# Performance work log

Hardware: AMD Instinct MI355X
Metric: run time of the kernel (lower is better)

Reference implementation:

```python
import jax, jax.numpy as jnp
import numpy as np

B, N, C, R = 4, 4096, 64, 16
EPS = 1e-12


def setup_inputs() -> dict:
    key = jax.random.key(0)
    k_x, k_w, k_u = jax.random.split(key, 3)
    x = jax.random.normal(k_x, (B, N, C), dtype=jnp.float32)
    W = jax.random.uniform(k_w, (B, N, N), dtype=jnp.float32)
    # lazily-initialized learnable low-rank factor U ~ 0.01 * randn(N, r)
    U = 0.01 * jax.random.normal(k_u, (N, R), dtype=jnp.float32)
    w_scale = jnp.asarray(1.0, dtype=jnp.float32)
    return {"x": x, "W": W, "U": U, "w_scale": w_scale}


def reference(x, W, U, w_scale):
    # symmetrize adjacency: W <- (W + W^T)/2
    Ws = 0.5 * (W + jnp.swapaxes(W, -1, -2))            # [B,N,N]
    # low-rank symmetric gate A = sigmoid(U U^T), shared over batch
    A = jax.nn.sigmoid(U @ U.T)                          # [N,N]
    K = Ws * A[None, :, :]                               # [B,N,N]
    # degree normalization K <- D^{-1/2} K D^{-1/2}
    # (diag_embed + two bmms in the original == row/col broadcast scaling)
    deg = jnp.maximum(K.sum(axis=-1), EPS)               # [B,N]
    d = jax.lax.rsqrt(deg)                               # [B,N]
    K = K * d[:, :, None] * d[:, None, :]                # [B,N,N]
    # coupling: w_scale * K @ x
    return w_scale * jnp.einsum('bnm,bmc->bnc', K, x)    # [B,N,C]
```

## Files before the change

### kernel.cpp

```cpp
#include <hip/hip_runtime.h>
#include <hip/hip_bf16.h>

#define B_ 4
#define N_ 4096
#define C_ 64
#define R_ 16
#define EPS_ 1e-12f

typedef __attribute__((ext_vector_type(8))) short bf16x8;
typedef __attribute__((ext_vector_type(4))) float f32x4;

static __device__ __forceinline__ unsigned short f2bf(float f) {
    unsigned int u = __float_as_uint(f);
    unsigned int r = (u + 0x7fffu + ((u >> 16) & 1u)) >> 16;
    return (unsigned short)r;
}
static __device__ __forceinline__ float bf2f(unsigned short us) {
    return __uint_as_float(((unsigned int)us) << 16);
}

static __device__ __forceinline__ size_t k0f_off(int b, int rt, int k32, int fq, int fr) {
    return ((((size_t)(b * 256 + rt)) * 128 + k32) * 4 + fq) * 128 + fr * 8;
}

__global__ __launch_bounds__(256) void k_pass1(
    const float* __restrict__ W, const float* __restrict__ U,
    unsigned short* __restrict__ K0, float* __restrict__ deg)
{
    const int tj = blockIdx.x, ti = blockIdx.y;
    if (ti > tj) return;
    const int I = ti * 64, J = tj * 64;
    const bool diag = (ti == tj);
    const int t = threadIdx.x;
    const int ii = t >> 2, g = t & 3, jjg = g * 16;

    __shared__ float UJ[64][17];
    __shared__ float Wc[64][65];
    __shared__ __align__(16) unsigned short K0s[64][72];

    {
        const float4 v = *(const float4*)(U + (size_t)(J + (t >> 2)) * R_ + (t & 3) * 4);
        UJ[t >> 2][(t & 3) * 4 + 0] = v.x;
        UJ[t >> 2][(t & 3) * 4 + 1] = v.y;
        UJ[t >> 2][(t & 3) * 4 + 2] = v.z;
        UJ[t >> 2][(t & 3) * 4 + 3] = v.w;
    }

    float4 wcv[4], wrv[4], wcvN[4], wrvN[4];
    #pragma unroll
    for (int k = 0; k < 4; k++) {
        const int idx = t + 256 * k, row = idx >> 4, c4 = idx & 15;
        wcv[k] = *(const float4*)(W + ((size_t)(0 * N_ + J + row)) * N_ + I + c4 * 4);
    }
    #pragma unroll
    for (int h = 0; h < 4; h++)
        wrv[h] = *(const float4*)(W + ((size_t)(0 * N_ + I + ii)) * N_ + J + jjg + 4 * h);

    float ui[16];
    {
        const float* up = U + (size_t)(I + ii) * R_;
        #pragma unroll
        for (int h = 0; h < 4; h++) {
            float4 v = *(const float4*)(up + 4 * h);
            ui[4*h] = v.x; ui[4*h+1] = v.y; ui[4*h+2] = v.z; ui[4*h+3] = v.w;
        }
    }
    __syncthreads();

    float a[16];
    #pragma unroll
    for (int q = 0; q < 16; q++) {
        float s = 0.f;
        #pragma unroll
        for (int k = 0; k < 16; k++) s += ui[k] * UJ[jjg + q][k];
        a[q] = 1.0f / (1.0f + __expf(-s));
    }

    #pragma unroll
    for (int k = 0; k < 4; k++) {
        const int idx = t + 256 * k, row = idx >> 4, c4 = idx & 15;
        Wc[row][c4*4+0] = wcv[k].x; Wc[row][c4*4+1] = wcv[k].y;
        Wc[row][c4*4+2] = wcv[k].z; Wc[row][c4*4+3] = wcv[k].w;
    }
    __syncthreads();

    for (int b = 0; b < B_; b++) {
        if (b < B_ - 1) {
            #pragma unroll
            for (int k = 0; k < 4; k++) {
                const int idx = t + 256 * k, row = idx >> 4, c4 = idx & 15;
                wcvN[k] = *(const float4*)(W + ((size_t)((b+1) * N_ + J + row)) * N_ + I + c4 * 4);
            }
            #pragma unroll
            for (int h = 0; h < 4; h++)
                wrvN[h] = *(const float4*)(W + ((size_t)((b+1) * N_ + I + ii)) * N_ + J + jjg + 4 * h);
        }

        const float* wrf = (const float*)wrv;
        float sumI = 0.f;
        unsigned int pk[8];
        #pragma unroll
        for (int q = 0; q < 16; q++) {
            float k0 = 0.5f * (wrf[q] + Wc[jjg + q][ii]) * a[q];
            sumI += k0;
            unsigned short us = f2bf(k0);
            if (q & 1) pk[q >> 1] |= ((unsigned int)us) << 16;
            else       pk[q >> 1] = us;
        }
        *(int4*)(&K0s[ii][jjg])     = make_int4(pk[0], pk[1], pk[2], pk[3]);
        *(int4*)(&K0s[ii][jjg + 8]) = make_int4(pk[4], pk[5], pk[6], pk[7]);
        {
            const int rt  = (I + ii) >> 4, fr = ii & 15;
            const int k32 = (J >> 5) + (g >> 1), fqa = (g & 1) * 2;
            unsigned short* dst = K0 + k0f_off(b, rt, k32, fqa, fr);
            *(int4*)(dst)       = make_int4(pk[0], pk[1], pk[2], pk[3]);
            *(int4*)(dst + 128) = make_int4(pk[4], pk[5], pk[6], pk[7]);
        }
        {
            float s = sumI + __shfl_xor(sumI, 1, 64);
            s += __shfl_xor(s, 2, 64);
            if (g == 0) atomicAdd(deg + b * N_ + I + ii, s);
        }
        __syncthreads();

        if (!diag) {
            const int c2 = t & 31, r8 = t >> 5;
            unsigned int v[8];
            float cs0 = 0.f, cs1 = 0.f;
            #pragma unroll
            for (int k = 0; k < 8; k++) {
                v[k] = *(const unsigned int*)(&K0s[r8 * 8 + k][c2 * 2]);
                cs0 += bf2f((unsigned short)(v[k] & 0xffffu));
                cs1 += bf2f((unsigned short)(v[k] >> 16));
            }
            unsigned int plo[4], phi[4];
            #pragma unroll
            for (int m = 0; m < 4; m++) {
                plo[m] = (v[2*m] & 0xffffu) | (v[2*m+1] << 16);
                phi[m] = (v[2*m] >> 16) | (v[2*m+1] & 0xffff0000u);
            }
            const int rtp  = (J >> 4) + (c2 >> 3), fr0 = (2 * c2) & 15;
            const int k32p = (I >> 5) + (r8 >> 2), fqp = r8 & 3;
            unsigned short* dst0 = K0 + k0f_off(b, rtp, k32p, fqp, fr0);
            *(int4*)(dst0)     = make_int4(plo[0], plo[1], plo[2], plo[3]);
            *(int4*)(dst0 + 8) = make_int4(phi[0], phi[1], phi[2], phi[3]);
            cs0 += __shfl_xor(cs0, 32, 64);
            cs1 += __shfl_xor(cs1, 32, 64);
            if ((t & 32) == 0) {
                atomicAdd(deg + b * N_ + J + 2 * c2,     cs0);
                atomicAdd(deg + b * N_ + J + 2 * c2 + 1, cs1);
            }
        }
        if (b < B_ - 1) {
            #pragma unroll
            for (int k = 0; k < 4; k++) {
                const int idx = t + 256 * k, row = idx >> 4, c4 = idx & 15;
                Wc[row][c4*4+0] = wcvN[k].x; Wc[row][c4*4+1] = wcvN[k].y;
                Wc[row][c4*4+2] = wcvN[k].z; Wc[row][c4*4+3] = wcvN[k].w;
            }
            #pragma unroll
            for (int h = 0; h < 4; h++) wrv[h] = wrvN[h];
            __syncthreads();
        }
    }
}

__global__ __launch_bounds__(256) void k_xdT(
    const float* __restrict__ x, const float* __restrict__ deg,
    unsigned short* __restrict__ xdT)
{
    const int jt = blockIdx.x, b = blockIdx.y;
    const int J = jt * 64, t = threadIdx.x;
    __shared__ float xt[64][69];
    #pragma unroll
    for (int k = 0; k < 4; k++) {
        int idx = t + 256 * k;
        int row = idx >> 4, f4 = idx & 15;
        float d = rsqrtf(fmaxf(deg[b * N_ + J + row], EPS_));
        float4 v = *(const float4*)(x + ((size_t)(b * N_ + J + row)) * C_ + f4 * 4);
        xt[row][f4*4+0] = v.x * d; xt[row][f4*4+1] = v.y * d;
        xt[row][f4*4+2] = v.z * d; xt[row][f4*4+3] = v.w * d;
    }
    __syncthreads();
    #pragma unroll
    for (int p = 0; p < 2; p++) {
        const int linear = p * 256 + t;
        const int k32h = linear >> 8, rem = linear & 255;
        const int cg = rem >> 6, l = rem & 63, fq = l >> 4, fr = l & 15;
        const int c = cg * 16 + fr;
        const int jb = k32h * 32 + fq * 8;
        unsigned int pk[4];
        #pragma unroll
        for (int m = 0; m < 4; m++) {
            pk[m] = (unsigned int)f2bf(xt[jb + 2*m][c]) |
                    ((unsigned int)f2bf(xt[jb + 2*m + 1][c]) << 16);
        }
        unsigned short* dst = xdT +
            (((size_t)(b * 128 + (J >> 5) + k32h)) * 4 + cg) * 512 + l * 8;
        *(int4*)dst = make_int4(pk[0], pk[1], pk[2], pk[3]);
    }
}

static __device__ __forceinline__ void gll16(const unsigned short* g, const unsigned short* l) {
    __builtin_amdgcn_global_load_lds(
        (const __attribute__((address_space(1))) unsigned int*)g,
        (__attribute__((address_space(3))) unsigned int*)l,
        16, 0, 0);
}

__global__ __launch_bounds__(256, 2) void k_gemm(
    const unsigned short* __restrict__ K0, const unsigned short* __restrict__ xdT,
    const float* __restrict__ deg, const float* __restrict__ wsc_p,
    float* __restrict__ out)
{
    const int mg = blockIdx.x, b = blockIdx.y;
    const int t = threadIdx.x, w = t >> 6, lane = t & 63;
    const int rt0 = mg * 2;
    const int rtl = w & 1, cgp = (w >> 1) * 2;
    const int fq = lane >> 4, fr = lane & 15;
    const int rt = rt0 + rtl;

    __shared__ __align__(16) unsigned short As[2 * 8 * 512];
    __shared__ __align__(16) unsigned short Bs[2 * 16 * 512];

    const float wsc = wsc_p[0];
    float dsc[4];
    #pragma unroll
    for (int r = 0; r < 4; r++)
        dsc[r] = wsc * rsqrtf(fmaxf(deg[b * N_ + rt * 16 + fq * 4 + r], EPS_));

    const unsigned short* gp[6];
    const unsigned short* lp[6];
    int ginc[6], linc[6];
    #pragma unroll
    for (int j = 0; j < 6; j++) {
        const int id = w * 6 + j;
        if (id < 8) {
            const int art = id >> 2, c = id & 3;
            gp[j] = K0 + (((size_t)(b * 256 + rt0 + art)) * 128 + c) * 512 + lane * 8;
            lp[j] = As + id * 512;
            ginc[j] = 4 * 512;
            linc[j] = 8 * 512;
        } else {
            const int bi = id - 8, kc = bi >> 2, cg = bi & 3;
            gp[j] = xdT + (((size_t)(b * 128 + kc)) * 4 + cg) * 512 + lane * 8;
            lp[j] = Bs + bi * 512;
            ginc[j] = 4 * 2048;
            linc[j] = 16 * 512;
        }
    }

    asm volatile("s_waitcnt vmcnt(0)" ::: "memory");
    __builtin_amdgcn_sched_barrier(0);

    #pragma unroll
    for (int j = 0; j < 6; j++) {
        gll16(gp[j], lp[j]);
        gp[j] += ginc[j];
    }

    f32x4 acc0 = {0.f,0.f,0.f,0.f}, acc1 = {0.f,0.f,0.f,0.f};
    const int lo = lane * 8;
    int cur = 0;

    for (int t4 = 0; t4 < 32; t4++) {
        if (t4 < 31) {
            #pragma unroll
            for (int j = 0; j < 6; j++) {
                gll16(gp[j], lp[j] + (cur ? 0 : linc[j]));
                gp[j] += ginc[j];
            }
        }
        __builtin_amdgcn_sched_barrier(0);
        if (t4 < 31) asm volatile("s_waitcnt vmcnt(6)" ::: "memory");
        else         asm volatile("s_waitcnt vmcnt(0)" ::: "memory");
        __builtin_amdgcn_s_barrier();
        __builtin_amdgcn_sched_barrier(0);

        const unsigned short* Ab = As + (cur ? 8 * 512 : 0) + rtl * 4 * 512 + lo;
        const unsigned short* Bb = Bs + (cur ? 16 * 512 : 0) + cgp * 512 + lo;
        #pragma unroll
        for (int c = 0; c < 4; c++) {
            bf16x8 av = *(const bf16x8*)(Ab + c * 512);
            bf16x8 b0 = *(const bf16x8*)(Bb + c * 2048);
            bf16x8 b1 = *(const bf16x8*)(Bb + c * 2048 + 512);
            acc0 = __builtin_amdgcn_mfma_f32_16x16x32_bf16(av, b0, acc0, 0, 0, 0);
            acc1 = __builtin_amdgcn_mfma_f32_16x16x32_bf16(av, b1, acc1, 0, 0, 0);
        }
        __builtin_amdgcn_sched_barrier(0);
        __builtin_amdgcn_s_barrier();
        cur ^= 1;
    }

    #pragma unroll
    for (int r = 0; r < 4; r++) {
        const int row = rt * 16 + fq * 4 + r;
        float* op = out + ((size_t)(b * N_ + row)) * C_;
        op[cgp * 16 + fr]      = dsc[r] * acc0[r];
        op[cgp * 16 + 16 + fr] = dsc[r] * acc1[r];
    }
}

extern "C" void kernel_launch(void* const* d_in, const int* in_sizes, int n_in,
                              void* d_out, int out_size, void* d_ws, size_t ws_size,
                              hipStream_t stream)
{
    const float* x   = (const float*)d_in[0];
    const float* W   = (const float*)d_in[1];
    const float* U   = (const float*)d_in[2];
    const float* wsc = (const float*)d_in[3];
    float* out = (float*)d_out;

    unsigned short* K0  = (unsigned short*)d_ws;
    float*          deg = (float*)((char*)d_ws + (size_t)B_ * N_ * N_ * 2);
    unsigned short* xdT = (unsigned short*)((char*)deg + (size_t)B_ * N_ * 4);

    hipMemsetAsync(deg, 0, (size_t)B_ * N_ * sizeof(float), stream);
    hipLaunchKernelGGL(k_pass1, dim3(64, 64), dim3(256), 0, stream, W, U, K0, deg);
    hipLaunchKernelGGL(k_xdT,  dim3(64, 4),   dim3(256), 0, stream, x, deg, xdT);
    hipLaunchKernelGGL(k_gemm, dim3(128, 4),  dim3(256), 0, stream, K0, xdT, deg, wsc, out);
}
```

Before: 444.8 us.

## Launch only upper-triangle tiles and double-buffer shared tiles to drop a barrier

Replaces the 64x64 grid with early-exiting lower-triangle blocks by a linear grid of 2080 blocks, mapped to (ti,tj) via a triangular index inversion. The transposed W tile in shared memory becomes bf16 and is double-buffered along with the K0 staging tile, so the next batch's tile is written before the single barrier and the second per-iteration __syncthreads is removed. The aims are less wasted block scheduling, fewer barriers per batch and a smaller shared footprint that allows higher occupancy. The trade-off is that the transposed W values are rounded to bf16 before symmetrization, adding some precision loss.

```diff
diff --git a/kernel.cpp b/kernel.cpp
--- a/kernel.cpp
+++ b/kernel.cpp
@@ -27,16 +27,20 @@
     const float* __restrict__ W, const float* __restrict__ U,
     unsigned short* __restrict__ K0, float* __restrict__ deg)
 {
-    const int tj = blockIdx.x, ti = blockIdx.y;
-    if (ti > tj) return;
+    const int lin = blockIdx.x;
+    float ff = 64.5f - sqrtf(64.5f * 64.5f - 2.0f * (float)lin);
+    int ti = (int)ff;
+    while ((ti + 1) * (129 - (ti + 1)) / 2 <= lin) ti++;
+    while (ti * (129 - ti) / 2 > lin) ti--;
+    const int tj = ti + (lin - ti * (129 - ti) / 2);
     const int I = ti * 64, J = tj * 64;
     const bool diag = (ti == tj);
     const int t = threadIdx.x;
     const int ii = t >> 2, g = t & 3, jjg = g * 16;
 
     __shared__ float UJ[64][17];
-    __shared__ float Wc[64][65];
-    __shared__ __align__(16) unsigned short K0s[64][72];
+    __shared__ unsigned short Wc[2][64][66];
+    __shared__ __align__(16) unsigned short K0s[2][64][72];
 
     {
         const float4 v = *(const float4*)(U + (size_t)(J + (t >> 2)) * R_ + (t & 3) * 4);
@@ -79,12 +83,15 @@
     #pragma unroll
     for (int k = 0; k < 4; k++) {
         const int idx = t + 256 * k, row = idx >> 4, c4 = idx & 15;
-        Wc[row][c4*4+0] = wcv[k].x; Wc[row][c4*4+1] = wcv[k].y;
-        Wc[row][c4*4+2] = wcv[k].z; Wc[row][c4*4+3] = wcv[k].w;
+        unsigned int d0 = (unsigned int)f2bf(wcv[k].x) | ((unsigned int)f2bf(wcv[k].y) << 16);
+        unsigned int d1 = (unsigned int)f2bf(wcv[k].z) | ((unsigned int)f2bf(wcv[k].w) << 16);
+        *(unsigned int*)&Wc[0][row][c4 * 4]     = d0;
+        *(unsigned int*)&Wc[0][row][c4 * 4 + 2] = d1;
     }
     __syncthreads();
 
     for (int b = 0; b < B_; b++) {
+        const int cur = b & 1;
         if (b < B_ - 1) {
             #pragma unroll
             for (int k = 0; k < 4; k++) {
@@ -101,14 +108,14 @@
         unsigned int pk[8];
         #pragma unroll
         for (int q = 0; q < 16; q++) {
-            float k0 = 0.5f * (wrf[q] + Wc[jjg + q][ii]) * a[q];
+            float k0 = 0.5f * (wrf[q] + bf2f(Wc[cur][jjg + q][ii])) * a[q];
             sumI += k0;
             unsigned short us = f2bf(k0);
             if (q & 1) pk[q >> 1] |= ((unsigned int)us) << 16;
             else       pk[q >> 1] = us;
         }
-        *(int4*)(&K0s[ii][jjg])     = make_int4(pk[0], pk[1], pk[2], pk[3]);
-        *(int4*)(&K0s[ii][jjg + 8]) = make_int4(pk[4], pk[5], pk[6], pk[7]);
+        *(int4*)(&K0s[cur][ii][jjg])     = make_int4(pk[0], pk[1], pk[2], pk[3]);
+        *(int4*)(&K0s[cur][ii][jjg + 8]) = make_int4(pk[4], pk[5], pk[6], pk[7]);
         {
             const int rt  = (I + ii) >> 4, fr = ii & 15;
             const int k32 = (J >> 5) + (g >> 1), fqa = (g & 1) * 2;
@@ -121,6 +128,18 @@
             s += __shfl_xor(s, 2, 64);
             if (g == 0) atomicAdd(deg + b * N_ + I + ii, s);
         }
+        if (b < B_ - 1) {
+            #pragma unroll
+            for (int k = 0; k < 4; k++) {
+                const int idx = t + 256 * k, row = idx >> 4, c4 = idx & 15;
+                unsigned int d0 = (unsigned int)f2bf(wcvN[k].x) | ((unsigned int)f2bf(wcvN[k].y) << 16);
+                unsigned int d1 = (unsigned int)f2bf(wcvN[k].z) | ((unsigned int)f2bf(wcvN[k].w) << 16);
+                *(unsigned int*)&Wc[cur ^ 1][row][c4 * 4]     = d0;
+                *(unsigned int*)&Wc[cur ^ 1][row][c4 * 4 + 2] = d1;
+            }
+            #pragma unroll
+            for (int h = 0; h < 4; h++) wrv[h] = wrvN[h];
+        }
         __syncthreads();
 
         if (!diag) {
@@ -129,7 +148,7 @@
             float cs0 = 0.f, cs1 = 0.f;
             #pragma unroll
             for (int k = 0; k < 8; k++) {
-                v[k] = *(const unsigned int*)(&K0s[r8 * 8 + k][c2 * 2]);
+                v[k] = *(const unsigned int*)(&K0s[cur][r8 * 8 + k][c2 * 2]);
                 cs0 += bf2f((unsigned short)(v[k] & 0xffffu));
                 cs1 += bf2f((unsigned short)(v[k] >> 16));
             }
@@ -150,17 +169,6 @@
                 atomicAdd(deg + b * N_ + J + 2 * c2,     cs0);
                 atomicAdd(deg + b * N_ + J + 2 * c2 + 1, cs1);
             }
-        }
-        if (b < B_ - 1) {
-            #pragma unroll
-            for (int k = 0; k < 4; k++) {
-                const int idx = t + 256 * k, row = idx >> 4, c4 = idx & 15;
-                Wc[row][c4*4+0] = wcvN[k].x; Wc[row][c4*4+1] = wcvN[k].y;
-                Wc[row][c4*4+2] = wcvN[k].z; Wc[row][c4*4+3] = wcvN[k].w;
-            }
-            #pragma unroll
-            for (int h = 0; h < 4; h++) wrv[h] = wrvN[h];
-            __syncthreads();
         }
     }
 }
@@ -316,7 +324,7 @@
     unsigned short* xdT = (unsigned short*)((char*)deg + (size_t)B_ * N_ * 4);
 
     hipMemsetAsync(deg, 0, (size_t)B_ * N_ * sizeof(float), stream);
-    hipLaunchKernelGGL(k_pass1, dim3(64, 64), dim3(256), 0, stream, W, U, K0, deg);
+    hipLaunchKernelGGL(k_pass1, dim3(2080), dim3(256), 0, stream, W, U, K0, deg);
     hipLaunchKernelGGL(k_xdT,  dim3(64, 4),   dim3(256), 0, stream, x, deg, xdT);
     hipLaunchKernelGGL(k_gemm, dim3(128, 4),  dim3(256), 0, stream, K0, xdT, deg, wsc, out);
 }
```

Measured after the change: 434.4 us. 1.02x faster.
